# Kernel tuning notes

Hardware: AMD Instinct MI355X
Metric: run time of the kernel (lower is better)

Reference implementation:

```python
import jax, jax.numpy as jnp
import numpy as np

N, D = 65536, 1024
EPS = 1e-12  # matches torch F.normalize default eps

def setup_inputs() -> dict:
    key = jax.random.key(0)
    k1, k2 = jax.random.split(key)
    premise = jax.random.normal(k1, (N, D), dtype=jnp.float32)
    hypothesis = jax.random.normal(k2, (N, D), dtype=jnp.float32)
    return {"premise": premise, "hypothesis": hypothesis}

def _l2_normalize(x):
    # torch.nn.functional.normalize(p=2, dim=-1): x / max(||x||, eps)
    norm = jnp.sqrt(jnp.sum(x * x, axis=-1, keepdims=True))
    return x / jnp.maximum(norm, EPS)

def reference(premise, hypothesis):
    # handle the [N,3,D] flattening branch of the original
    if premise.ndim == 3 and hypothesis.ndim == 3 and premise.shape[1] == 3 and hypothesis.shape[1] == 3:
        premise = premise.reshape(premise.shape[0], -1)
        hypothesis = hypothesis.reshape(hypothesis.shape[0], -1)
    p = _l2_normalize(premise)
    h = _l2_normalize(hypothesis)
    # diag(p @ h.T) == per-row dot product; avoid materializing NxN matrix
    return jnp.sum(p * h, axis=-1)
```

## Files before the change

kernel.cpp:

```cpp
#include <hip/hip_runtime.h>
#include <hip/hip_bf16.h>

#define D 1024
#define WAVES_PER_BLOCK 4

__global__ __launch_bounds__(256) void CosineSimilarity_76785425318088_kernel(
    const float* __restrict__ premise,
    const float* __restrict__ hypothesis,
    float* __restrict__ out,
    int n_rows) {
    const int wave = threadIdx.x >> 6;
    const int lane = threadIdx.x & 63;
    const int row = blockIdx.x * WAVES_PER_BLOCK + wave;
    if (row >= n_rows) return;

    const float4* __restrict__ prow = reinterpret_cast<const float4*>(premise    + (size_t)row * D);
    const float4* __restrict__ hrow = reinterpret_cast<const float4*>(hypothesis + (size_t)row * D);

    float dot = 0.f, pp = 0.f, hh = 0.f;
    #pragma unroll
    for (int j = 0; j < D / 4 / 64; ++j) {
        float4 a = prow[j * 64 + lane];
        float4 b = hrow[j * 64 + lane];
        dot = fmaf(a.x, b.x, dot); dot = fmaf(a.y, b.y, dot);
        dot = fmaf(a.z, b.z, dot); dot = fmaf(a.w, b.w, dot);
        pp  = fmaf(a.x, a.x, pp);  pp  = fmaf(a.y, a.y, pp);
        pp  = fmaf(a.z, a.z, pp);  pp  = fmaf(a.w, a.w, pp);
        hh  = fmaf(b.x, b.x, hh);  hh  = fmaf(b.y, b.y, hh);
        hh  = fmaf(b.z, b.z, hh);  hh  = fmaf(b.w, b.w, hh);
    }

    #pragma unroll
    for (int off = 32; off > 0; off >>= 1) {
        dot += __shfl_down(dot, off, 64);
        pp  += __shfl_down(pp,  off, 64);
        hh  += __shfl_down(hh,  off, 64);
    }

    if (lane == 0) {
        const float eps = 1e-12f;
        float denom = fmaxf(sqrtf(pp), eps) * fmaxf(sqrtf(hh), eps);
        out[row] = dot / denom;
    }
}

extern "C" void kernel_launch(void* const* d_in, const int* in_sizes, int n_in,
                              void* d_out, int out_size, void* d_ws, size_t ws_size,
                              hipStream_t stream) {
    const float* premise    = (const float*)d_in[0];
    const float* hypothesis = (const float*)d_in[1];
    float* out = (float*)d_out;
    const int n_rows = out_size;

    const int blocks = (n_rows + WAVES_PER_BLOCK - 1) / WAVES_PER_BLOCK;
    CosineSimilarity_76785425318088_kernel<<<blocks, 256, 0, stream>>>(
        premise, hypothesis, out, n_rows);
}
```

Baseline: 491.7 us.

## Use persistent grid-stride waves processing two rows each

Replaces one-wave-per-row launch with a fixed grid of 2048 blocks where each wave loops over rows in a grid stride, handling two rows per iteration. This is meant to cut block launch overhead and put more loads in flight per wave to hide memory latency. Handling two rows per wave assumes an even row count, so an odd count would read past the end. It also raises register use.

```diff
diff --git a/kernel.cpp b/kernel.cpp
--- a/kernel.cpp
+++ b/kernel.cpp
@@ -2,45 +2,62 @@
 #include <hip/hip_bf16.h>
 
 #define D 1024
-#define WAVES_PER_BLOCK 4
+#define BLOCK 256
+#define GRID 2048
 
-__global__ __launch_bounds__(256) void CosineSimilarity_76785425318088_kernel(
+__global__ __launch_bounds__(BLOCK) void CosineSimilarity_76785425318088_kernel(
     const float* __restrict__ premise,
     const float* __restrict__ hypothesis,
     float* __restrict__ out,
     int n_rows) {
-    const int wave = threadIdx.x >> 6;
     const int lane = threadIdx.x & 63;
-    const int row = blockIdx.x * WAVES_PER_BLOCK + wave;
-    if (row >= n_rows) return;
+    const int wave_global = (blockIdx.x * BLOCK + threadIdx.x) >> 6;
+    const int n_waves = (GRID * BLOCK) >> 6;
+    const float eps = 1e-12f;
 
-    const float4* __restrict__ prow = reinterpret_cast<const float4*>(premise    + (size_t)row * D);
-    const float4* __restrict__ hrow = reinterpret_cast<const float4*>(hypothesis + (size_t)row * D);
+    for (int row = wave_global * 2; row < n_rows; row += n_waves * 2) {
+        const float4* __restrict__ p0 = reinterpret_cast<const float4*>(premise    + (size_t)row * D);
+        const float4* __restrict__ h0 = reinterpret_cast<const float4*>(hypothesis + (size_t)row * D);
+        const float4* __restrict__ p1 = reinterpret_cast<const float4*>(premise    + (size_t)(row + 1) * D);
+        const float4* __restrict__ h1 = reinterpret_cast<const float4*>(hypothesis + (size_t)(row + 1) * D);
 
-    float dot = 0.f, pp = 0.f, hh = 0.f;
-    #pragma unroll
-    for (int j = 0; j < D / 4 / 64; ++j) {
-        float4 a = prow[j * 64 + lane];
-        float4 b = hrow[j * 64 + lane];
-        dot = fmaf(a.x, b.x, dot); dot = fmaf(a.y, b.y, dot);
-        dot = fmaf(a.z, b.z, dot); dot = fmaf(a.w, b.w, dot);
-        pp  = fmaf(a.x, a.x, pp);  pp  = fmaf(a.y, a.y, pp);
-        pp  = fmaf(a.z, a.z, pp);  pp  = fmaf(a.w, a.w, pp);
-        hh  = fmaf(b.x, b.x, hh);  hh  = fmaf(b.y, b.y, hh);
-        hh  = fmaf(b.z, b.z, hh);  hh  = fmaf(b.w, b.w, hh);
-    }
+        float d0 = 0.f, pp0 = 0.f, hh0 = 0.f;
+        float d1 = 0.f, pp1 = 0.f, hh1 = 0.f;
 
-    #pragma unroll
-    for (int off = 32; off > 0; off >>= 1) {
-        dot += __shfl_down(dot, off, 64);
-        pp  += __shfl_down(pp,  off, 64);
-        hh  += __shfl_down(hh,  off, 64);
-    }
+        #pragma unroll
+        for (int j = 0; j < D / 4 / 64; ++j) {
+            float4 a0 = p0[j * 64 + lane];
+            float4 b0 = h0[j * 64 + lane];
+            float4 a1 = p1[j * 64 + lane];
+            float4 b1 = h1[j * 64 + lane];
+            d0  = fmaf(a0.x, b0.x, d0);  d0  = fmaf(a0.y, b0.y, d0);
+            d0  = fmaf(a0.z, b0.z, d0);  d0  = fmaf(a0.w, b0.w, d0);
+            pp0 = fmaf(a0.x, a0.x, pp0); pp0 = fmaf(a0.y, a0.y, pp0);
+            pp0 = fmaf(a0.z, a0.z, pp0); pp0 = fmaf(a0.w, a0.w, pp0);
+            hh0 = fmaf(b0.x, b0.x, hh0); hh0 = fmaf(b0.y, b0.y, hh0);
+            hh0 = fmaf(b0.z, b0.z, hh0); hh0 = fmaf(b0.w, b0.w, hh0);
+            d1  = fmaf(a1.x, b1.x, d1);  d1  = fmaf(a1.y, b1.y, d1);
+            d1  = fmaf(a1.z, b1.z, d1);  d1  = fmaf(a1.w, b1.w, d1);
+            pp1 = fmaf(a1.x, a1.x, pp1); pp1 = fmaf(a1.y, a1.y, pp1);
+            pp1 = fmaf(a1.z, a1.z, pp1); pp1 = fmaf(a1.w, a1.w, pp1);
+            hh1 = fmaf(b1.x, b1.x, hh1); hh1 = fmaf(b1.y, b1.y, hh1);
+            hh1 = fmaf(b1.z, b1.z, hh1); hh1 = fmaf(b1.w, b1.w, hh1);
+        }
 
-    if (lane == 0) {
-        const float eps = 1e-12f;
-        float denom = fmaxf(sqrtf(pp), eps) * fmaxf(sqrtf(hh), eps);
-        out[row] = dot / denom;
+        #pragma unroll
+        for (int off = 32; off > 0; off >>= 1) {
+            d0  += __shfl_down(d0,  off, 64);
+            pp0 += __shfl_down(pp0, off, 64);
+            hh0 += __shfl_down(hh0, off, 64);
+            d1  += __shfl_down(d1,  off, 64);
+            pp1 += __shfl_down(pp1, off, 64);
+            hh1 += __shfl_down(hh1, off, 64);
+        }
+
+        if (lane == 0) {
+            out[row]     = d0 / (fmaxf(sqrtf(pp0), eps) * fmaxf(sqrtf(hh0), eps));
+            out[row + 1] = d1 / (fmaxf(sqrtf(pp1), eps) * fmaxf(sqrtf(hh1), eps));
+        }
     }
 }
 
@@ -52,7 +69,6 @@
     float* out = (float*)d_out;
     const int n_rows = out_size;
 
-    const int blocks = (n_rows + WAVES_PER_BLOCK - 1) / WAVES_PER_BLOCK;
-    CosineSimilarity_76785425318088_kernel<<<blocks, 256, 0, stream>>>(
+    CosineSimilarity_76785425318088_kernel<<<GRID, BLOCK, 0, stream>>>(
         premise, hypothesis, out, n_rows);
 }
```

Result: no change. 499.2 us (+1.5%).
